# Performance work log

Measured on AMD Instinct MI355X. Metric: run time of the kernel, lower is better.

Reference implementation:

```python
import jax, jax.numpy as jnp
import numpy as np

N_NODES = 100000
N_EDGES = 1600000
IN_DIM = 128
HID = 256
OUT_DIM = 1
NUM_GRAPHS = 2048


def setup_inputs() -> dict:
    key = jax.random.key(0)
    ks = jax.random.split(key, 12)
    x = jax.random.normal(ks[0], (N_NODES, IN_DIM), dtype=jnp.float32)
    edge_index = jax.random.randint(ks[1], (2, N_EDGES), 0, N_NODES, dtype=jnp.int32)
    batch = jnp.sort(jax.random.randint(ks[2], (N_NODES,), 0, NUM_GRAPHS, dtype=jnp.int32))
    def glorot(k, shape):
        lim = float(np.sqrt(6.0 / (shape[0] + shape[1])))
        return jax.random.uniform(k, shape, jnp.float32, -lim, lim)
    W1 = glorot(ks[3], (IN_DIM, HID));  b1 = jnp.zeros((HID,), jnp.float32)
    W2 = glorot(ks[4], (HID, HID));     b2 = jnp.zeros((HID,), jnp.float32)
    Wf1 = glorot(ks[5], (HID, HID // 2)); bf1 = jnp.zeros((HID // 2,), jnp.float32)
    Wf2 = glorot(ks[6], (HID // 2, OUT_DIM)); bf2 = jnp.zeros((OUT_DIM,), jnp.float32)
    return {"x": x, "edge_index": edge_index, "batch": batch,
            "W1": W1, "b1": b1, "W2": W2, "b2": b2,
            "Wf1": Wf1, "bf1": bf1, "Wf2": Wf2, "bf2": bf2}


def _gcn_conv(x, W, b, src, dst, norm, num_nodes):
    # PyG GCNConv: h = X W; out[dst] += norm_e * h[src]; out += b
    h = x @ W                                   # [N, F]
    msg = h[src] * norm[:, None]                # [E', F] gather + scale
    agg = jax.ops.segment_sum(msg, dst, num_segments=num_nodes)
    return agg + b


def reference(x, edge_index, batch, W1, b1, W2, b2, Wf1, bf1, Wf2, bf2):
    n = x.shape[0]
    loop = jnp.arange(n, dtype=edge_index.dtype)
    src = jnp.concatenate([edge_index[0], loop])  # add self-loops (GCN default)
    dst = jnp.concatenate([edge_index[1], loop])
    # symmetric normalization: deg over A+I at dst index
    deg = jax.ops.segment_sum(jnp.ones_like(src, dtype=x.dtype), dst, num_segments=n)
    dinv = jnp.where(deg > 0, jax.lax.rsqrt(deg), 0.0)
    norm = dinv[src] * dinv[dst]                 # [E']

    h = jax.nn.relu(_gcn_conv(x, W1, b1, src, dst, norm, n))
    h = jax.nn.relu(_gcn_conv(h, W2, b2, src, dst, norm, n))

    # global_mean_pool over graphs
    sums = jax.ops.segment_sum(h, batch, num_segments=NUM_GRAPHS)
    cnts = jax.ops.segment_sum(jnp.ones((n,), h.dtype), batch, num_segments=NUM_GRAPHS)
    pooled = sums / jnp.maximum(cnts, 1.0)[:, None]   # [G, HID]

    out = jax.nn.relu(pooled @ Wf1 + bf1) @ Wf2 + bf2  # [G, OUT_DIM]
    return out
```

## Files before the change

### kernel.cpp

```cpp
#include <hip/hip_runtime.h>
#include <hip/hip_bf16.h>

#define N_NODES 100000
#define N_EDGES 1600000
#define IN_DIM 128
#define HID 256
#define NUM_GRAPHS 2048
#define M_PAD 100096
#define SCAN_BLOCKS 98

typedef __bf16 bf16x8 __attribute__((ext_vector_type(8)));
typedef float f32x4 __attribute__((ext_vector_type(4)));

__device__ inline unsigned short f2bf(float x) {
    union { __hip_bfloat16 h; unsigned short u; } v;
    v.h = __float2bfloat16(x);
    return v.u;
}
__device__ inline float bf2f(unsigned short u) {
    return __uint_as_float(((unsigned int)u) << 16);
}
__device__ inline int rfl(int x) { return __builtin_amdgcn_readfirstlane(x); }

__global__ void count_deg_kernel(const int* __restrict__ ei, int* __restrict__ deg) {
    int e = blockIdx.x * blockDim.x + threadIdx.x;
    if (e < N_EDGES) {
        atomicAdd(&deg[ei[N_EDGES + e]], 1);
    }
}

__global__ __launch_bounds__(1024) void blocksum_kernel(const int* __restrict__ deg,
                                                        int* __restrict__ bsum,
                                                        float* __restrict__ dinv) {
    int i = blockIdx.x * 1024 + threadIdx.x;
    int v = (i < N_NODES) ? deg[i] : 0;
    if (i < N_NODES) dinv[i] = rsqrtf((float)(v + 1));
    __shared__ int s[1024];
    int t = threadIdx.x;
    s[t] = v;
    __syncthreads();
#pragma unroll
    for (int off = 512; off > 0; off >>= 1) {
        if (t < off) s[t] += s[t + off];
        __syncthreads();
    }
    if (t == 0) bsum[blockIdx.x] = s[0];
}

__global__ __launch_bounds__(128) void bscan_kernel(int* __restrict__ bsum) {
    __shared__ int s[128];
    int t = threadIdx.x;
    int v = (t < SCAN_BLOCKS) ? bsum[t] : 0;
    s[t] = v;
    __syncthreads();
#pragma unroll
    for (int off = 1; off < 128; off <<= 1) {
        int x = (t >= off) ? s[t - off] : 0;
        __syncthreads();
        s[t] += x;
        __syncthreads();
    }
    if (t < SCAN_BLOCKS) bsum[t] = (t > 0) ? s[t - 1] : 0;
}

__global__ __launch_bounds__(1024) void scanout_kernel(const int* __restrict__ deg,
                                                       const int* __restrict__ bsum,
                                                       int* __restrict__ rowptr) {
    int i = blockIdx.x * 1024 + threadIdx.x;
    int t = threadIdx.x;
    int v = (i < N_NODES) ? deg[i] : 0;
    __shared__ int s[1024];
    s[t] = v;
    __syncthreads();
#pragma unroll
    for (int off = 1; off < 1024; off <<= 1) {
        int x = (t >= off) ? s[t - off] : 0;
        __syncthreads();
        s[t] += x;
        __syncthreads();
    }
    int base = bsum[blockIdx.x];
    int excl = (t > 0) ? s[t - 1] : 0;
    if (i < N_NODES) rowptr[i] = base + excl;
    if (i == N_NODES - 1) rowptr[N_NODES] = base + s[t];
}

__global__ void fill_kernel(const int* __restrict__ ei, const int* __restrict__ rowptr,
                            int* __restrict__ fill, int* __restrict__ esrc) {
    int e = blockIdx.x * blockDim.x + threadIdx.x;
    if (e < N_EDGES) {
        int dst = ei[N_EDGES + e];
        int pos = rowptr[dst] + atomicAdd(&fill[dst], 1);
        esrc[pos] = ei[e];
    }
}

__global__ void x2bf_kernel(const float* __restrict__ x, unsigned short* __restrict__ xb) {
    size_t i = ((size_t)blockIdx.x * 256 + threadIdx.x) * 4;
    float4 v = *(const float4*)(x + i);
    ushort4 o;
    o.x = f2bf(v.x); o.y = f2bf(v.y); o.z = f2bf(v.z); o.w = f2bf(v.w);
    *(ushort4*)(xb + i) = o;
}

__global__ void wsplit_all_kernel(const float* __restrict__ W1, const float* __restrict__ W2,
                                  unsigned short* __restrict__ W1th, unsigned short* __restrict__ W1tl,
                                  unsigned short* __restrict__ W2th, unsigned short* __restrict__ W2tl) {
    int idx = blockIdx.x * 256 + threadIdx.x;
    if (idx < IN_DIM * 256) {
        int k = idx >> 8, n = idx & 255;
        float w = W1[idx];
        unsigned short h = f2bf(w);
        unsigned short l = f2bf(w - bf2f(h));
        W1th[n * IN_DIM + k] = h;
        W1tl[n * IN_DIM + k] = l;
    } else {
        int i2 = idx - IN_DIM * 256;
        int k = i2 >> 8, n = i2 & 255;
        float w = W2[i2];
        unsigned short h = f2bf(w);
        unsigned short l = f2bf(w - bf2f(h));
        W2th[n * HID + k] = h;
        W2tl[n * HID + k] = l;
    }
}

template <int K, bool ASPLIT>
__global__ __launch_bounds__(256, 3) void fused_layer(const unsigned short* __restrict__ X,
                                                      const int* __restrict__ esrc,
                                                      const int* __restrict__ rowptr,
                                                      const float* __restrict__ dinv,
                                                      const unsigned short* __restrict__ Bh,
                                                      const unsigned short* __restrict__ Bl,
                                                      const float* __restrict__ bias,
                                                      unsigned short* __restrict__ Cout) {
    constexpr int ROWB = K * 2;
    __shared__ __align__(16) unsigned char lds[(ASPLIT ? 2 : 1) * 64 * ROWB];
    unsigned char* AhsB = lds;
    unsigned char* AlsB = lds + 64 * ROWB;

    int tid = threadIdx.x;
    int wid = tid >> 6, lane = tid & 63;
    int bm = blockIdx.x * 64;

    for (int i = 0; i < 16; i++) {
        int r = wid * 16 + i;
        int node = rfl(bm + r);
        if constexpr (K == 128) {
            float2 acc = make_float2(0.f, 0.f);
            if (node < N_NODES) {
                float ddst = dinv[node];
                int s = rfl(rowptr[node]);
                int e = rfl(rowptr[node + 1]);
                float w0 = ddst * ddst;
                ushort2 h0 = *((const ushort2*)(X + (size_t)node * 128) + lane);
                acc.x = w0 * bf2f(h0.x);
                acc.y = w0 * bf2f(h0.y);
                int j = s;
                for (; j + 8 <= e; j += 8) {
                    int si[8];
#pragma unroll
                    for (int u = 0; u < 8; u++) si[u] = rfl(esrc[j + u]);
                    ushort2 xv[8];
#pragma unroll
                    for (int u = 0; u < 8; u++)
                        xv[u] = *((const ushort2*)(X + (size_t)si[u] * 128) + lane);
                    float a[8];
#pragma unroll
                    for (int u = 0; u < 8; u++) a[u] = dinv[si[u]] * ddst;
#pragma unroll
                    for (int u = 0; u < 8; u++) {
                        acc.x = fmaf(a[u], bf2f(xv[u].x), acc.x);
                        acc.y = fmaf(a[u], bf2f(xv[u].y), acc.y);
                    }
                }
                for (; j + 4 <= e; j += 4) {
                    int si[4];
#pragma unroll
                    for (int u = 0; u < 4; u++) si[u] = rfl(esrc[j + u]);
                    ushort2 xv[4];
#pragma unroll
                    for (int u = 0; u < 4; u++)
                        xv[u] = *((const ushort2*)(X + (size_t)si[u] * 128) + lane);
                    float a[4];
#pragma unroll
                    for (int u = 0; u < 4; u++) a[u] = dinv[si[u]] * ddst;
#pragma unroll
                    for (int u = 0; u < 4; u++) {
                        acc.x = fmaf(a[u], bf2f(xv[u].x), acc.x);
                        acc.y = fmaf(a[u], bf2f(xv[u].y), acc.y);
                    }
                }
                for (; j < e; j++) {
                    int src = rfl(esrc[j]);
                    float w = dinv[src] * ddst;
                    ushort2 xv = *((const ushort2*)(X + (size_t)src * 128) + lane);
                    acc.x = fmaf(w, bf2f(xv.x), acc.x);
                    acc.y = fmaf(w, bf2f(xv.y), acc.y);
                }
            }
            unsigned bo = ((unsigned)(r * 256 + lane * 4)) ^ (((unsigned)(r & 7)) << 4);
            ushort2 hi, lo;
            hi.x = f2bf(acc.x); lo.x = f2bf(acc.x - bf2f(hi.x));
            hi.y = f2bf(acc.y); lo.y = f2bf(acc.y - bf2f(hi.y));
            *(ushort2*)(AhsB + bo) = hi;
            if (ASPLIT) *(ushort2*)(AlsB + bo) = lo;
        } else {
            float4 acc = make_float4(0.f, 0.f, 0.f, 0.f);
            if (node < N_NODES) {
                float ddst = dinv[node];
                int s = rfl(rowptr[node]);
                int e = rfl(rowptr[node + 1]);
                float w0 = ddst * ddst;
                ushort4 h0 = *((const ushort4*)(X + (size_t)node * 256) + lane);
                acc.x = w0 * bf2f(h0.x);
                acc.y = w0 * bf2f(h0.y);
                acc.z = w0 * bf2f(h0.z);
                acc.w = w0 * bf2f(h0.w);
                int j = s;
                for (; j + 8 <= e; j += 8) {
                    int si[8];
#pragma unroll
                    for (int u = 0; u < 8; u++) si[u] = rfl(esrc[j + u]);
                    ushort4 xv[8];
#pragma unroll
                    for (int u = 0; u < 8; u++)
                        xv[u] = *((const ushort4*)(X + (size_t)si[u] * 256) + lane);
                    float a[8];
#pragma unroll
                    for (int u = 0; u < 8; u++) a[u] = dinv[si[u]] * ddst;
#pragma unroll
                    for (int u = 0; u < 8; u++) {
                        acc.x = fmaf(a[u], bf2f(xv[u].x), acc.x);
                        acc.y = fmaf(a[u], bf2f(xv[u].y), acc.y);
                        acc.z = fmaf(a[u], bf2f(xv[u].z), acc.z);
                        acc.w = fmaf(a[u], bf2f(xv[u].w), acc.w);
                    }
                }
                for (; j + 4 <= e; j += 4) {
                    int si[4];
#pragma unroll
                    for (int u = 0; u < 4; u++) si[u] = rfl(esrc[j + u]);
                    ushort4 xv[4];
#pragma unroll
                    for (int u = 0; u < 4; u++)
                        xv[u] = *((const ushort4*)(X + (size_t)si[u] * 256) + lane);
                    float a[4];
#pragma unroll
                    for (int u = 0; u < 4; u++) a[u] = dinv[si[u]] * ddst;
#pragma unroll
                    for (int u = 0; u < 4; u++) {
                        acc.x = fmaf(a[u], bf2f(xv[u].x), acc.x);
                        acc.y = fmaf(a[u], bf2f(xv[u].y), acc.y);
                        acc.z = fmaf(a[u], bf2f(xv[u].z), acc.z);
                        acc.w = fmaf(a[u], bf2f(xv[u].w), acc.w);
                    }
                }
                for (; j < e; j++) {
                    int src = rfl(esrc[j]);
                    float w = dinv[src] * ddst;
                    ushort4 xv = *((const ushort4*)(X + (size_t)src * 256) + lane);
                    acc.x = fmaf(w, bf2f(xv.x), acc.x);
                    acc.y = fmaf(w, bf2f(xv.y), acc.y);
                    acc.z = fmaf(w, bf2f(xv.z), acc.z);
                    acc.w = fmaf(w, bf2f(xv.w), acc.w);
                }
            }
            unsigned bo = ((unsigned)(r * 512 + lane * 8)) ^ (((unsigned)(r & 7)) << 4);
            ushort4 hi;
            hi.x = f2bf(acc.x); hi.y = f2bf(acc.y);
            hi.z = f2bf(acc.z); hi.w = f2bf(acc.w);
            *(ushort4*)(AhsB + bo) = hi;
        }
    }
    __syncthreads();

    int lrow = lane & 15, quad = lane >> 4;
    f32x4 acc[4][4];
#pragma unroll
    for (int mi = 0; mi < 4; mi++)
#pragma unroll
        for (int ni = 0; ni < 4; ni++) acc[mi][ni] = (f32x4){0.f, 0.f, 0.f, 0.f};

#pragma unroll
    for (int k0 = 0; k0 < K; k0 += 32) {
        bf16x8 ah[4], al[4];
#pragma unroll
        for (int mi = 0; mi < 4; mi++) {
            int r = mi * 16 + lrow;
            unsigned bo = ((unsigned)(r * ROWB + (k0 + quad * 8) * 2)) ^ (((unsigned)(r & 7)) << 4);
            ah[mi] = *(const bf16x8*)(AhsB + bo);
            if (ASPLIT) al[mi] = *(const bf16x8*)(AlsB + bo);
        }
#pragma unroll
        for (int ni = 0; ni < 4; ni++) {
            int rowB = wid * 64 + ni * 16 + lrow;
            size_t gb = (size_t)rowB * K + k0 + quad * 8;
            bf16x8 bh = *(const bf16x8*)(Bh + gb);
            bf16x8 bl = *(const bf16x8*)(Bl + gb);
#pragma unroll
            for (int mi = 0; mi < 4; mi++) {
                acc[mi][ni] = __builtin_amdgcn_mfma_f32_16x16x32_bf16(ah[mi], bh, acc[mi][ni], 0, 0, 0);
                acc[mi][ni] = __builtin_amdgcn_mfma_f32_16x16x32_bf16(ah[mi], bl, acc[mi][ni], 0, 0, 0);
                if (ASPLIT)
                    acc[mi][ni] = __builtin_amdgcn_mfma_f32_16x16x32_bf16(al[mi], bh, acc[mi][ni], 0, 0, 0);
            }
        }
    }

    float bv[4];
#pragma unroll
    for (int ni = 0; ni < 4; ni++) bv[ni] = bias[wid * 64 + ni * 16 + lrow];
#pragma unroll
    for (int mi = 0; mi < 4; mi++) {
        int row0 = bm + mi * 16 + quad * 4;
#pragma unroll
        for (int ni = 0; ni < 4; ni++) {
            int col = wid * 64 + ni * 16 + lrow;
#pragma unroll
            for (int rr = 0; rr < 4; rr++) {
                int row = row0 + rr;
                if (row < N_NODES) {
                    float v = fmaxf(acc[mi][ni][rr] + bv[ni], 0.f);
                    Cout[(size_t)row * 256 + col] = f2bf(v);
                }
            }
        }
    }
}

__global__ __launch_bounds__(256) void pool_mlp_kernel(const unsigned short* __restrict__ h,
                                                       const int* __restrict__ batch,
                                                       const float* __restrict__ Wf1,
                                                       const float* __restrict__ bf1,
                                                       const float* __restrict__ Wf2,
                                                       const float* __restrict__ bf2,
                                                       float* __restrict__ out) {
    int g = blockIdx.x;
    int t = threadIdx.x;
    __shared__ int bounds[2];
    if (t < 2) {
        int target = g + t;
        int lo = 0, hi = N_NODES;
        while (lo < hi) {
            int mid = (lo + hi) >> 1;
            if (batch[mid] < target) lo = mid + 1;
            else hi = mid;
        }
        bounds[t] = lo;
    }
    __syncthreads();
    int lo = bounds[0], hi = bounds[1];

    float acc = 0.f;
    for (int n = lo; n < hi; n++) acc += bf2f(h[(size_t)n * HID + t]);
    float inv = (hi > lo) ? 1.0f / (float)(hi - lo) : 0.f;
    __shared__ float p[256];
    p[t] = acc * inv;
    __syncthreads();

    float hv = 0.f;
    if (t < 128) {
        float a = bf1[t];
#pragma unroll 8
        for (int k = 0; k < 256; k++) a = fmaf(p[k], Wf1[k * 128 + t], a);
        hv = fmaxf(a, 0.f) * Wf2[t];
    }
#pragma unroll
    for (int off = 32; off > 0; off >>= 1) hv += __shfl_down(hv, off, 64);
    __shared__ float partial[4];
    if ((t & 63) == 0) partial[t >> 6] = hv;
    __syncthreads();
    if (t == 0) out[g] = partial[0] + partial[1] + bf2[0];
}

extern "C" void kernel_launch(void* const* d_in, const int* in_sizes, int n_in,
                              void* d_out, int out_size, void* d_ws, size_t ws_size,
                              hipStream_t stream) {
    const float* x   = (const float*)d_in[0];
    const int*   ei  = (const int*)d_in[1];
    const int*   bat = (const int*)d_in[2];
    const float* W1  = (const float*)d_in[3];
    const float* b1  = (const float*)d_in[4];
    const float* W2  = (const float*)d_in[5];
    const float* b2  = (const float*)d_in[6];
    const float* Wf1 = (const float*)d_in[7];
    const float* bf1 = (const float*)d_in[8];
    const float* Wf2 = (const float*)d_in[9];
    const float* bf2 = (const float*)d_in[10];
    float* out = (float*)d_out;

    char* ws = (char*)d_ws;
    int*   deg    = (int*)(ws);
    float* dinv   = (float*)(ws + 0x0080000);
    int*   rowptr = (int*)(ws + 0x0100000);
    int*   fill   = (int*)(ws + 0x0180000);
    int*   bsum   = (int*)(ws + 0x01F0000);
    int*   esrc   = (int*)(ws + 0x0200000);
    unsigned short* W1th = (unsigned short*)(ws + 0x0820000);
    unsigned short* W1tl = (unsigned short*)(ws + 0x0830000);
    unsigned short* W2th = (unsigned short*)(ws + 0x0840000);
    unsigned short* W2tl = (unsigned short*)(ws + 0x0860000);
    unsigned short* xbf  = (unsigned short*)(ws + 0x0880000);
    unsigned short* H1bf = (unsigned short*)(ws + 0x2100000);
    unsigned short* H2bf = (unsigned short*)(ws + 0x5200000);
    (void)ws_size;

    hipMemsetAsync(deg, 0, (size_t)N_NODES * sizeof(int), stream);
    hipMemsetAsync(fill, 0, (size_t)N_NODES * sizeof(int), stream);

    x2bf_kernel<<<(N_NODES * IN_DIM / 4) / 256, 256, 0, stream>>>(x, xbf);
    wsplit_all_kernel<<<((IN_DIM + HID) * 256) / 256, 256, 0, stream>>>(W1, W2, W1th, W1tl, W2th, W2tl);

    count_deg_kernel<<<(N_EDGES + 255) / 256, 256, 0, stream>>>(ei, deg);
    blocksum_kernel<<<SCAN_BLOCKS, 1024, 0, stream>>>(deg, bsum, dinv);
    bscan_kernel<<<1, 128, 0, stream>>>(bsum);
    scanout_kernel<<<SCAN_BLOCKS, 1024, 0, stream>>>(deg, bsum, rowptr);
    fill_kernel<<<(N_EDGES + 255) / 256, 256, 0, stream>>>(ei, rowptr, fill, esrc);

    fused_layer<IN_DIM, true><<<M_PAD / 64, 256, 0, stream>>>(xbf, esrc, rowptr, dinv,
                                                              W1th, W1tl, b1, H1bf);

    fused_layer<HID, false><<<M_PAD / 64, 256, 0, stream>>>(H1bf, esrc, rowptr, dinv,
                                                            W2th, W2tl, b2, H2bf);

    pool_mlp_kernel<<<NUM_GRAPHS, 256, 0, stream>>>(H2bf, bat, Wf1, bf1, Wf2, bf2, out);
}
```

Baseline: 636.8 us.

## Split fused aggregate+GEMM layers into separate aggregation and MFMA GEMM kernels

```diff
diff --git a/kernel.cpp b/kernel.cpp
--- a/kernel.cpp
+++ b/kernel.cpp
@@ -125,187 +125,208 @@
     }
 }
 
+__global__ __launch_bounds__(256) void agg128_kernel(const unsigned short* __restrict__ X,
+                                                     const int* __restrict__ esrc,
+                                                     const int* __restrict__ rowptr,
+                                                     const float* __restrict__ dinv,
+                                                     unsigned short* __restrict__ Ah,
+                                                     unsigned short* __restrict__ Al) {
+    int node = rfl(blockIdx.x * 4 + (threadIdx.x >> 6));
+    int lane = threadIdx.x & 63;
+    float ddst = dinv[node];
+    int s = rfl(rowptr[node]);
+    int e = rfl(rowptr[node + 1]);
+
+    float w0 = ddst * ddst;
+    ushort2 h0 = *((const ushort2*)(X + (size_t)node * 128) + lane);
+    float2 acc = make_float2(w0 * bf2f(h0.x), w0 * bf2f(h0.y));
+
+    int j = s;
+    for (; j + 8 <= e; j += 8) {
+        int si[8];
+#pragma unroll
+        for (int u = 0; u < 8; u++) si[u] = rfl(esrc[j + u]);
+        ushort2 xv[8];
+#pragma unroll
+        for (int u = 0; u < 8; u++)
+            xv[u] = *((const ushort2*)(X + (size_t)si[u] * 128) + lane);
+        float a[8];
+#pragma unroll
+        for (int u = 0; u < 8; u++) a[u] = dinv[si[u]] * ddst;
+#pragma unroll
+        for (int u = 0; u < 8; u++) {
+            acc.x = fmaf(a[u], bf2f(xv[u].x), acc.x);
+            acc.y = fmaf(a[u], bf2f(xv[u].y), acc.y);
+        }
+    }
+    for (; j + 4 <= e; j += 4) {
+        int si[4];
+#pragma unroll
+        for (int u = 0; u < 4; u++) si[u] = rfl(esrc[j + u]);
+        ushort2 xv[4];
+#pragma unroll
+        for (int u = 0; u < 4; u++)
+            xv[u] = *((const ushort2*)(X + (size_t)si[u] * 128) + lane);
+        float a[4];
+#pragma unroll
+        for (int u = 0; u < 4; u++) a[u] = dinv[si[u]] * ddst;
+#pragma unroll
+        for (int u = 0; u < 4; u++) {
+            acc.x = fmaf(a[u], bf2f(xv[u].x), acc.x);
+            acc.y = fmaf(a[u], bf2f(xv[u].y), acc.y);
+        }
+    }
+    for (; j < e; j++) {
+        int src = rfl(esrc[j]);
+        float w = dinv[src] * ddst;
+        ushort2 xv = *((const ushort2*)(X + (size_t)src * 128) + lane);
+        acc.x = fmaf(w, bf2f(xv.x), acc.x);
+        acc.y = fmaf(w, bf2f(xv.y), acc.y);
+    }
+    size_t o = (size_t)node * 128 + lane * 2;
+    ushort2 hi, lo;
+    hi.x = f2bf(acc.x); lo.x = f2bf(acc.x - bf2f(hi.x));
+    hi.y = f2bf(acc.y); lo.y = f2bf(acc.y - bf2f(hi.y));
+    *(ushort2*)(Ah + o) = hi;
+    *(ushort2*)(Al + o) = lo;
+}
+
+__global__ __launch_bounds__(256) void agg256_kernel(const unsigned short* __restrict__ H,
+                                                     const int* __restrict__ esrc,
+                                                     const int* __restrict__ rowptr,
+                                                     const float* __restrict__ dinv,
+                                                     unsigned short* __restrict__ Ah) {
+    int node = rfl(blockIdx.x * 4 + (threadIdx.x >> 6));
+    int lane = threadIdx.x & 63;
+    float ddst = dinv[node];
+    int s = rfl(rowptr[node]);
+    int e = rfl(rowptr[node + 1]);
+
+    float w0 = ddst * ddst;
+    ushort4 h0 = *((const ushort4*)(H + (size_t)node * 256) + lane);
+    float4 acc = make_float4(w0 * bf2f(h0.x), w0 * bf2f(h0.y),
+                             w0 * bf2f(h0.z), w0 * bf2f(h0.w));
+
+    int j = s;
+    for (; j + 8 <= e; j += 8) {
+        int si[8];
+#pragma unroll
+        for (int u = 0; u < 8; u++) si[u] = rfl(esrc[j + u]);
+        ushort4 xv[8];
+#pragma unroll
+        for (int u = 0; u < 8; u++)
+            xv[u] = *((const ushort4*)(H + (size_t)si[u] * 256) + lane);
+        float a[8];
+#pragma unroll
+        for (int u = 0; u < 8; u++) a[u] = dinv[si[u]] * ddst;
+#pragma unroll
+        for (int u = 0; u < 8; u++) {
+            acc.x = fmaf(a[u], bf2f(xv[u].x), acc.x);
+            acc.y = fmaf(a[u], bf2f(xv[u].y), acc.y);
+            acc.z = fmaf(a[u], bf2f(xv[u].z), acc.z);
+            acc.w = fmaf(a[u], bf2f(xv[u].w), acc.w);
+        }
+    }
+    for (; j + 4 <= e; j += 4) {
+        int si[4];
+#pragma unroll
+        for (int u = 0; u < 4; u++) si[u] = rfl(esrc[j + u]);
+        ushort4 xv[4];
+#pragma unroll
+        for (int u = 0; u < 4; u++)
+            xv[u] = *((const ushort4*)(H + (size_t)si[u] * 256) + lane);
+        float a[4];
+#pragma unroll
+        for (int u = 0; u < 4; u++) a[u] = dinv[si[u]] * ddst;
+#pragma unroll
+        for (int u = 0; u < 4; u++) {
+            acc.x = fmaf(a[u], bf2f(xv[u].x), acc.x);
+            acc.y = fmaf(a[u], bf2f(xv[u].y), acc.y);
+            acc.z = fmaf(a[u], bf2f(xv[u].z), acc.z);
+            acc.w = fmaf(a[u], bf2f(xv[u].w), acc.w);
+        }
+    }
+    for (; j < e; j++) {
+        int src = rfl(esrc[j]);
+        float w = dinv[src] * ddst;
+        ushort4 xv = *((const ushort4*)(H + (size_t)src * 256) + lane);
+        acc.x = fmaf(w, bf2f(xv.x), acc.x);
+        acc.y = fmaf(w, bf2f(xv.y), acc.y);
+        acc.z = fmaf(w, bf2f(xv.z), acc.z);
+        acc.w = fmaf(w, bf2f(xv.w), acc.w);
+    }
+    size_t o = (size_t)node * 256 + lane * 4;
+    ushort4 hi;
+    hi.x = f2bf(acc.x); hi.y = f2bf(acc.y);
+    hi.z = f2bf(acc.z); hi.w = f2bf(acc.w);
+    *(ushort4*)(Ah + o) = hi;
+}
+
 template <int K, bool ASPLIT>
-__global__ __launch_bounds__(256, 3) void fused_layer(const unsigned short* __restrict__ X,
-                                                      const int* __restrict__ esrc,
-                                                      const int* __restrict__ rowptr,
-                                                      const float* __restrict__ dinv,
-                                                      const unsigned short* __restrict__ Bh,
-                                                      const unsigned short* __restrict__ Bl,
-                                                      const float* __restrict__ bias,
-                                                      unsigned short* __restrict__ Cout) {
-    constexpr int ROWB = K * 2;
-    __shared__ __align__(16) unsigned char lds[(ASPLIT ? 2 : 1) * 64 * ROWB];
+__global__ __launch_bounds__(256, 3) void mfma_gemm_bias_relu(const unsigned short* __restrict__ Ah,
+                                                              const unsigned short* __restrict__ Al,
+                                                              const unsigned short* __restrict__ Bh,
+                                                              const unsigned short* __restrict__ Bl,
+                                                              const float* __restrict__ bias,
+                                                              unsigned short* __restrict__ Cout) {
+    __shared__ __align__(16) unsigned char lds[(ASPLIT ? 2 : 1) * 4096];
     unsigned char* AhsB = lds;
-    unsigned char* AlsB = lds + 64 * ROWB;
+    unsigned char* AlsB = lds + 4096;
 
     int tid = threadIdx.x;
     int wid = tid >> 6, lane = tid & 63;
+    int lrow = lane & 15, quad = lane >> 4;
     int bm = blockIdx.x * 64;
 
-    for (int i = 0; i < 16; i++) {
-        int r = wid * 16 + i;
-        int node = rfl(bm + r);
-        if constexpr (K == 128) {
-            float2 acc = make_float2(0.f, 0.f);
-            if (node < N_NODES) {
-                float ddst = dinv[node];
-                int s = rfl(rowptr[node]);
-                int e = rfl(rowptr[node + 1]);
-                float w0 = ddst * ddst;
-                ushort2 h0 = *((const ushort2*)(X + (size_t)node * 128) + lane);
-                acc.x = w0 * bf2f(h0.x);
-                acc.y = w0 * bf2f(h0.y);
-                int j = s;
-                for (; j + 8 <= e; j += 8) {
-                    int si[8];
-#pragma unroll
-                    for (int u = 0; u < 8; u++) si[u] = rfl(esrc[j + u]);
-                    ushort2 xv[8];
-#pragma unroll
-                    for (int u = 0; u < 8; u++)
-                        xv[u] = *((const ushort2*)(X + (size_t)si[u] * 128) + lane);
-                    float a[8];
-#pragma unroll
-                    for (int u = 0; u < 8; u++) a[u] = dinv[si[u]] * ddst;
-#pragma unroll
-                    for (int u = 0; u < 8; u++) {
-                        acc.x = fmaf(a[u], bf2f(xv[u].x), acc.x);
-                        acc.y = fmaf(a[u], bf2f(xv[u].y), acc.y);
-                    }
-                }
-                for (; j + 4 <= e; j += 4) {
-                    int si[4];
-#pragma unroll
-                    for (int u = 0; u < 4; u++) si[u] = rfl(esrc[j + u]);
-                    ushort2 xv[4];
-#pragma unroll
-                    for (int u = 0; u < 4; u++)
-                        xv[u] = *((const ushort2*)(X + (size_t)si[u] * 128) + lane);
-                    float a[4];
-#pragma unroll
-                    for (int u = 0; u < 4; u++) a[u] = dinv[si[u]] * ddst;
-#pragma unroll
-                    for (int u = 0; u < 4; u++) {
-                        acc.x = fmaf(a[u], bf2f(xv[u].x), acc.x);
-                        acc.y = fmaf(a[u], bf2f(xv[u].y), acc.y);
-                    }
-                }
-                for (; j < e; j++) {
-                    int src = rfl(esrc[j]);
-                    float w = dinv[src] * ddst;
-                    ushort2 xv = *((const ushort2*)(X + (size_t)src * 128) + lane);
-                    acc.x = fmaf(w, bf2f(xv.x), acc.x);
-                    acc.y = fmaf(w, bf2f(xv.y), acc.y);
-                }
+    f32x4 acc[4][4];
+#pragma unroll
+    for (int mi = 0; mi < 4; mi++)
+#pragma unroll
+        for (int ni = 0; ni < 4; ni++) acc[mi][ni] = (f32x4){0.f, 0.f, 0.f, 0.f};
+
+    int srow = tid >> 2, spart = tid & 3;
+    unsigned sbo = ((unsigned)(srow * 64 + spart * 16)) ^ (((unsigned)(srow & 7)) << 4);
+
+    for (int k0 = 0; k0 < K; k0 += 32) {
+        {
+            size_t ga = (size_t)(bm + srow) * K + k0 + spart * 8;
+            ulonglong2 v = *(const ulonglong2*)(Ah + ga);
+            *(ulonglong2*)(AhsB + sbo) = v;
+            if (ASPLIT) {
+                ulonglong2 v2 = *(const ulonglong2*)(Al + ga);
+                *(ulonglong2*)(AlsB + sbo) = v2;
             }
-            unsigned bo = ((unsigned)(r * 256 + lane * 4)) ^ (((unsigned)(r & 7)) << 4);
-            ushort2 hi, lo;
-            hi.x = f2bf(acc.x); lo.x = f2bf(acc.x - bf2f(hi.x));
-            hi.y = f2bf(acc.y); lo.y = f2bf(acc.y - bf2f(hi.y));
-            *(ushort2*)(AhsB + bo) = hi;
-            if (ASPLIT) *(ushort2*)(AlsB + bo) = lo;
-        } else {
-            float4 acc = make_float4(0.f, 0.f, 0.f, 0.f);
-            if (node < N_NODES) {
-                float ddst = dinv[node];
-                int s = rfl(rowptr[node]);
-                int e = rfl(rowptr[node + 1]);
-                float w0 = ddst * ddst;
-                ushort4 h0 = *((const ushort4*)(X + (size_t)node * 256) + lane);
-                acc.x = w0 * bf2f(h0.x);
-                acc.y = w0 * bf2f(h0.y);
-                acc.z = w0 * bf2f(h0.z);
-                acc.w = w0 * bf2f(h0.w);
-                int j = s;
-                for (; j + 8 <= e; j += 8) {
-                    int si[8];
-#pragma unroll
-                    for (int u = 0; u < 8; u++) si[u] = rfl(esrc[j + u]);
-                    ushort4 xv[8];
-#pragma unroll
-                    for (int u = 0; u < 8; u++)
-                        xv[u] = *((const ushort4*)(X + (size_t)si[u] * 256) + lane);
-                    float a[8];
-#pragma unroll
-                    for (int u = 0; u < 8; u++) a[u] = dinv[si[u]] * ddst;
-#pragma unroll
-                    for (int u = 0; u < 8; u++) {
-                        acc.x = fmaf(a[u], bf2f(xv[u].x), acc.x);
-                        acc.y = fmaf(a[u], bf2f(xv[u].y), acc.y);
-                        acc.z = fmaf(a[u], bf2f(xv[u].z), acc.z);
-                        acc.w = fmaf(a[u], bf2f(xv[u].w), acc.w);
-                    }
-                }
-                for (; j + 4 <= e; j += 4) {
-                    int si[4];
-#pragma unroll
-                    for (int u = 0; u < 4; u++) si[u] = rfl(esrc[j + u]);
-                    ushort4 xv[4];
-#pragma unroll
-                    for (int u = 0; u < 4; u++)
-                        xv[u] = *((const ushort4*)(X + (size_t)si[u] * 256) + lane);
-                    float a[4];
-#pragma unroll
-                    for (int u = 0; u < 4; u++) a[u] = dinv[si[u]] * ddst;
-#pragma unroll
-                    for (int u = 0; u < 4; u++) {
-                        acc.x = fmaf(a[u], bf2f(xv[u].x), acc.x);
-                        acc.y = fmaf(a[u], bf2f(xv[u].y), acc.y);
-                        acc.z = fmaf(a[u], bf2f(xv[u].z), acc.z);
-                        acc.w = fmaf(a[u], bf2f(xv[u].w), acc.w);
-                    }
-                }
-                for (; j < e; j++) {
-                    int src = rfl(esrc[j]);
-                    float w = dinv[src] * ddst;
-                    ushort4 xv = *((const ushort4*)(X + (size_t)src * 256) + lane);
-                    acc.x = fmaf(w, bf2f(xv.x), acc.x);
-                    acc.y = fmaf(w, bf2f(xv.y), acc.y);
-                    acc.z = fmaf(w, bf2f(xv.z), acc.z);
-                    acc.w = fmaf(w, bf2f(xv.w), acc.w);
-                }
-            }
-            unsigned bo = ((unsigned)(r * 512 + lane * 8)) ^ (((unsigned)(r & 7)) << 4);
-            ushort4 hi;
-            hi.x = f2bf(acc.x); hi.y = f2bf(acc.y);
-            hi.z = f2bf(acc.z); hi.w = f2bf(acc.w);
-            *(ushort4*)(AhsB + bo) = hi;
-        }
-    }
-    __syncthreads();
-
-    int lrow = lane & 15, quad = lane >> 4;
-    f32x4 acc[4][4];
-#pragma unroll
-    for (int mi = 0; mi < 4; mi++)
-#pragma unroll
-        for (int ni = 0; ni < 4; ni++) acc[mi][ni] = (f32x4){0.f, 0.f, 0.f, 0.f};
-
-#pragma unroll
-    for (int k0 = 0; k0 < K; k0 += 32) {
-        bf16x8 ah[4], al[4];
-#pragma unroll
-        for (int mi = 0; mi < 4; mi++) {
-            int r = mi * 16 + lrow;
-            unsigned bo = ((unsigned)(r * ROWB + (k0 + quad * 8) * 2)) ^ (((unsigned)(r & 7)) << 4);
-            ah[mi] = *(const bf16x8*)(AhsB + bo);
-            if (ASPLIT) al[mi] = *(const bf16x8*)(AlsB + bo);
-        }
+        }
+        __syncthreads();
+
+        bf16x8 bh[4], bl[4];
 #pragma unroll
         for (int ni = 0; ni < 4; ni++) {
             int rowB = wid * 64 + ni * 16 + lrow;
             size_t gb = (size_t)rowB * K + k0 + quad * 8;
-            bf16x8 bh = *(const bf16x8*)(Bh + gb);
-            bf16x8 bl = *(const bf16x8*)(Bl + gb);
+            bh[ni] = *(const bf16x8*)(Bh + gb);
+            bl[ni] = *(const bf16x8*)(Bl + gb);
+        }
+
+        bf16x8 ah[4], al[4];
+#pragma unroll
+        for (int mi = 0; mi < 4; mi++) {
+            int r = mi * 16 + lrow;
+            unsigned bo = ((unsigned)(r * 64 + quad * 16)) ^ (((unsigned)(r & 7)) << 4);
+            ah[mi] = *(const bf16x8*)(AhsB + bo);
+            if (ASPLIT) al[mi] = *(const bf16x8*)(AlsB + bo);
+        }
+
+#pragma unroll
+        for (int ni = 0; ni < 4; ni++)
 #pragma unroll
             for (int mi = 0; mi < 4; mi++) {
-                acc[mi][ni] = __builtin_amdgcn_mfma_f32_16x16x32_bf16(ah[mi], bh, acc[mi][ni], 0, 0, 0);
-                acc[mi][ni] = __builtin_amdgcn_mfma_f32_16x16x32_bf16(ah[mi], bl, acc[mi][ni], 0, 0, 0);
+                acc[mi][ni] = __builtin_amdgcn_mfma_f32_16x16x32_bf16(ah[mi], bh[ni], acc[mi][ni], 0, 0, 0);
+                acc[mi][ni] = __builtin_amdgcn_mfma_f32_16x16x32_bf16(ah[mi], bl[ni], acc[mi][ni], 0, 0, 0);
                 if (ASPLIT)
-                    acc[mi][ni] = __builtin_amdgcn_mfma_f32_16x16x32_bf16(al[mi], bh, acc[mi][ni], 0, 0, 0);
+                    acc[mi][ni] = __builtin_amdgcn_mfma_f32_16x16x32_bf16(al[mi], bh[ni], acc[mi][ni], 0, 0, 0);
             }
-        }
+        __syncthreads();
     }
 
     float bv[4];
@@ -401,9 +422,12 @@
     unsigned short* W1tl = (unsigned short*)(ws + 0x0830000);
     unsigned short* W2th = (unsigned short*)(ws + 0x0840000);
     unsigned short* W2tl = (unsigned short*)(ws + 0x0860000);
-    unsigned short* xbf  = (unsigned short*)(ws + 0x0880000);
-    unsigned short* H1bf = (unsigned short*)(ws + 0x2100000);
-    unsigned short* H2bf = (unsigned short*)(ws + 0x5200000);
+    unsigned short* A1h  = (unsigned short*)(ws + 0x0880000);
+    unsigned short* A1l  = (unsigned short*)(ws + 0x20F0000);
+    unsigned short* A2   = (unsigned short*)(ws + 0x0880000);
+    unsigned short* xbf  = (unsigned short*)(ws + 0x6A40000);
+    unsigned short* H1bf = (unsigned short*)(ws + 0x6A40000);
+    unsigned short* H2bf = (unsigned short*)(ws + 0x6A40000);
     (void)ws_size;
 
     hipMemsetAsync(deg, 0, (size_t)N_NODES * sizeof(int), stream);
@@ -418,11 +442,11 @@
     scanout_kernel<<<SCAN_BLOCKS, 1024, 0, stream>>>(deg, bsum, rowptr);
     fill_kernel<<<(N_EDGES + 255) / 256, 256, 0, stream>>>(ei, rowptr, fill, esrc);
 
-    fused_layer<IN_DIM, true><<<M_PAD / 64, 256, 0, stream>>>(xbf, esrc, rowptr, dinv,
-                                                              W1th, W1tl, b1, H1bf);
-
-    fused_layer<HID, false><<<M_PAD / 64, 256, 0, stream>>>(H1bf, esrc, rowptr, dinv,
-                                                            W2th, W2tl, b2, H2bf);
+    agg128_kernel<<<N_NODES / 4, 256, 0, stream>>>(xbf, esrc, rowptr, dinv, A1h, A1l);
+    mfma_gemm_bias_relu<IN_DIM, true><<<M_PAD / 64, 256, 0, stream>>>(A1h, A1l, W1th, W1tl, b1, H1bf);
+
+    agg256_kernel<<<N_NODES / 4, 256, 0, stream>>>(H1bf, esrc, rowptr, dinv, A2);
+    mfma_gemm_bias_relu<HID, false><<<M_PAD / 64, 256, 0, stream>>>(A2, nullptr, W2th, W2tl, b2, H2bf);
 
     pool_mlp_kernel<<<NUM_GRAPHS, 256, 0, stream>>>(H2bf, bat, Wf1, bf1, Wf2, bf2, out);
 }
```

After: 632.0 us. About the same (-0.8%).
